# Kernel tuning notes

Measured on AMD Instinct MI355X. Metric: run time of the kernel, lower is better.

Reference implementation:

```python
import jax, jax.numpy as jnp
import numpy as np

FC = 8  # heads_count
EPS = 1e-12  # torch F.normalize eps


def setup_inputs() -> dict:
    key = jax.random.key(0)
    ks = jax.random.split(key, 8)
    n, l, s, C, H = 4, 4096, 256, 256, 256
    return {
        "x0": jax.random.normal(ks[0], (n, l, C), jnp.float32),
        "center1": jax.random.normal(ks[1], (n, s, C), jnp.float32),
        "W0": jax.random.normal(ks[2], (H, C), jnp.float32) * 0.05,
        "b0": jax.random.normal(ks[3], (H,), jnp.float32) * 0.05,
        "W1": jax.random.normal(ks[4], (2 * H, C), jnp.float32) * 0.05,
        "b1": jax.random.normal(ks[5], (2 * H,), jnp.float32) * 0.05,
        "Wm": jax.random.normal(ks[6], (C, H), jnp.float32) * 0.05,
        "bm": jax.random.normal(ks[7], (C,), jnp.float32) * 0.05,
        "alpha": jnp.ones((1,), jnp.float32),
        "beta": jnp.zeros((1,), jnp.float32),
    }


def _l2norm(x):
    # matches torch F.normalize(dim=-1): x / max(||x||, eps)
    nrm = jnp.sqrt(jnp.sum(x * x, axis=-1, keepdims=True))
    return x / jnp.maximum(nrm, EPS)


def reference(x0, center1, W0, b0, W1, b1, Wm, bm, alpha, beta):
    n, l, c = x0.shape
    s = center1.shape[1]
    H = W0.shape[0]
    sc = H // FC
    m = n * FC
    # projections
    x0p = x0 @ W0.T + b0                        # [n, l, H]
    c1 = center1 @ W1.T + b1                    # [n, s, 2H]
    # split heads: 'n l (fc sc) -> (n fc) l sc'
    x0p = x0p.reshape(n, l, FC, sc).transpose(0, 2, 1, 3).reshape(m, l, sc)
    c1 = c1.reshape(n, s, FC, 2 * sc).transpose(0, 2, 1, 3).reshape(m, s, 2 * sc)
    c_point, c_value = c1[..., :sc], c1[..., sc:]
    # cosine similarity + affine + sigmoid
    sim = jnp.einsum('mlc,msc->mls', _l2norm(x0p), _l2norm(c_point))
    sim = jax.nn.sigmoid(alpha[0] * sim + beta[0])
    # top-1 hard routing
    max_vals = jnp.max(sim, axis=2)             # [m, l]
    max_idx = jnp.argmax(sim, axis=2)           # [m, l]
    gathered = jnp.take_along_axis(c_value, max_idx[:, :, None], axis=1)  # [m, l, sc]
    dispatched = max_vals[:, :, None] * gathered
    # '(n fc) l sc -> n l (fc sc)'
    dispatched = dispatched.reshape(n, FC, l, sc).transpose(0, 2, 1, 3).reshape(n, l, H)
    return dispatched @ Wm.T + bm               # [n, l, c]
```

## Files before the change

### kernel.cpp

```cpp
#include <hip/hip_runtime.h>
#include <math.h>

#define Nn 4
#define Ll 4096
#define Ss 256
#define Cc 256
#define FC 8
#define SC 32

typedef __attribute__((ext_vector_type(8))) short short8;
typedef __attribute__((ext_vector_type(8))) _Float16 half8;
typedef __attribute__((ext_vector_type(4))) float f32x4;

__device__ __forceinline__ unsigned short f2bf(float x) {
  unsigned int u = __float_as_uint(x);
  return (unsigned short)((u + 0x7FFFu + ((u >> 16) & 1u)) >> 16);
}

__device__ __forceinline__ void split8v(float4 a, float4 b,
                                        half8& hi, half8& lo) {
  float v[8] = {a.x, a.y, a.z, a.w, b.x, b.y, b.z, b.w};
#pragma unroll
  for (int i = 0; i < 8; i++) {
    float x = v[i];
    _Float16 h = (_Float16)x;
    float r = (x - (float)h) * 2048.f;
    hi[i] = h;
    lo[i] = (_Float16)r;
  }
}

#define STAGE(Abuf, Bbuf, K0)                                               \
  {                                                                         \
    _Pragma("unroll")                                                       \
    for (int j = 0; j < 2; j++) {                                           \
      int c = wave * 2 + j;                                                 \
      const float* g = Ag + (m0blk + 8 * c + lr) * Cc + (K0) + scol;        \
      __builtin_amdgcn_global_load_lds(                                     \
          (const __attribute__((address_space(1))) void*)g,                 \
          (__attribute__((address_space(3))) void*)((Abuf) + c * 256),      \
          16, 0, 0);                                                        \
    }                                                                       \
    _Pragma("unroll")                                                       \
    for (int j = 0; j < 2; j++) {                                           \
      int c = wave * 2 + j;                                                 \
      const float* g =                                                      \
          Bg + (size_t)(n0blk + 8 * c + lr) * Cc + (K0) + scol;             \
      __builtin_amdgcn_global_load_lds(                                     \
          (const __attribute__((address_space(1))) void*)g,                 \
          (__attribute__((address_space(3))) void*)((Bbuf) + c * 256),      \
          16, 0, 0);                                                        \
    }                                                                       \
  }

#define KSTEP(Ac, Bc)                                                       \
  {                                                                         \
    half8 Bh[2], Bl[2];                                                     \
    _Pragma("unroll")                                                       \
    for (int ni = 0; ni < 2; ni++) {                                        \
      int rw = bR0 + ni * 16 + l15;                                         \
      int rb = rw * 32, xs = rw & 7;                                        \
      float4 f0 = *(const float4*)&(Bc)[rb + (((quad * 2) ^ xs) << 2)];     \
      float4 f1 = *(const float4*)&(Bc)[rb + (((quad * 2 + 1) ^ xs) << 2)]; \
      split8v(f0, f1, Bh[ni], Bl[ni]);                                      \
    }                                                                       \
    _Pragma("unroll")                                                       \
    for (int mi = 0; mi < 2; mi++) {                                        \
      int rw = aR0 + mi * 16 + l15;                                         \
      int rb = rw * 32, xs = rw & 7;                                        \
      float4 f0 = *(const float4*)&(Ac)[rb + (((quad * 2) ^ xs) << 2)];     \
      float4 f1 = *(const float4*)&(Ac)[rb + (((quad * 2 + 1) ^ xs) << 2)]; \
      half8 Ah, Al;                                                         \
      split8v(f0, f1, Ah, Al);                                              \
      _Pragma("unroll")                                                     \
      for (int ni = 0; ni < 2; ni++) {                                      \
        acc1[mi][ni] = __builtin_amdgcn_mfma_f32_16x16x32_f16(              \
            Ah, Bh[ni], acc1[mi][ni], 0, 0, 0);                             \
        acc2a[mi][ni] = __builtin_amdgcn_mfma_f32_16x16x32_f16(             \
            Ah, Bl[ni], acc2a[mi][ni], 0, 0, 0);                            \
        acc2b[mi][ni] = __builtin_amdgcn_mfma_f32_16x16x32_f16(             \
            Al, Bh[ni], acc2b[mi][ni], 0, 0, 0);                            \
      }                                                                     \
    }                                                                       \
  }

__global__ __launch_bounds__(256, 4) void proj_mfma_k(
    const float* __restrict__ x0, const float* __restrict__ W0,
    const float* __restrict__ b0, const float* __restrict__ center1,
    const float* __restrict__ W1, const float* __restrict__ b1,
    float* __restrict__ xn, float* __restrict__ cpn, float* __restrict__ cval) {
  __shared__ float As[2][64 * 32];
  __shared__ float Bs[2][64 * 32];
  int t = threadIdx.x;
  int wave = t >> 6, lane = t & 63;
  int quad = lane >> 4, l15 = lane & 15;
  int l8 = lane & 7, lr = lane >> 3;
  int scol = (l8 ^ lr) << 2;
  int b = blockIdx.x;

  const float *Ag, *Bg, *bias;
  size_t m0blk;
  int n0blk;
  bool isX = (b < 1024);
  if (isX) {
    int rt = b & 255, cb = b >> 8;
    m0blk = (size_t)rt * 64;
    n0blk = cb * 64;
    Ag = x0; Bg = W0; bias = b0;
  } else {
    int b2 = b - 1024;
    m0blk = (size_t)(b2 >> 3) * 64;
    n0blk = (b2 & 7) * 64;
    Ag = center1; Bg = W1; bias = b1;
  }

  int aR0 = (wave & 1) * 32;
  int bR0 = (wave >> 1) * 32;
  int n0w = n0blk + bR0;

  f32x4 acc1[2][2], acc2a[2][2], acc2b[2][2];
#pragma unroll
  for (int ni = 0; ni < 2; ni++) {
    float bv = bias[n0w + ni * 16 + l15];
    f32x4 ci = {bv, bv, bv, bv};
    f32x4 zz = {0.f, 0.f, 0.f, 0.f};
#pragma unroll
    for (int mi = 0; mi < 2; mi++) {
      acc1[mi][ni] = ci; acc2a[mi][ni] = zz; acc2b[mi][ni] = zz;
    }
  }

  float* Ac = &As[0][0]; float* An = &As[1][0];
  float* Bc = &Bs[0][0]; float* Bn = &Bs[1][0];
  STAGE(Ac, Bc, 0);
#pragma unroll 1
  for (int kt = 0; kt < 8; kt++) {
    if (kt < 7) {
      STAGE(An, Bn, (kt + 1) * 32);
      asm volatile("s_waitcnt vmcnt(4)" ::: "memory");
    } else {
      asm volatile("s_waitcnt vmcnt(0)" ::: "memory");
    }
    __builtin_amdgcn_sched_barrier(0);
    __builtin_amdgcn_s_barrier();
    __builtin_amdgcn_sched_barrier(0);
    KSTEP(Ac, Bc);
    asm volatile("s_waitcnt lgkmcnt(0)" ::: "memory");
    __builtin_amdgcn_sched_barrier(0);
    __builtin_amdgcn_s_barrier();
    __builtin_amdgcn_sched_barrier(0);
    float* tp;
    tp = Ac; Ac = An; An = tp;
    tp = Bc; Bc = Bn; Bn = tp;
  }

  size_t m0 = m0blk + aR0;
  if (isX) {
#pragma unroll
    for (int mi = 0; mi < 2; mi++) {
#pragma unroll
      for (int reg = 0; reg < 4; reg++) {
        size_t row = m0 + mi * 16 + quad * 4 + reg;
        float* orow = xn + row * Cc + n0w;
#pragma unroll
        for (int ni = 0; ni < 2; ni++)
          orow[ni * 16 + l15] =
              acc1[mi][ni][reg] +
              (acc2a[mi][ni][reg] + acc2b[mi][ni][reg]) * (1.f / 2048.f);
      }
    }
  } else {
    int f = n0w >> 6;
    bool point = (n0w & 32) == 0;
#pragma unroll
    for (int mi = 0; mi < 2; mi++) {
#pragma unroll
      for (int reg = 0; reg < 4; reg++) {
        int row = (int)m0 + mi * 16 + quad * 4 + reg;
        int nI = row >> 8, s = row & 255;
        float v0 = acc1[mi][0][reg] +
                   (acc2a[mi][0][reg] + acc2b[mi][0][reg]) * (1.f / 2048.f);
        float v1 = acc1[mi][1][reg] +
                   (acc2a[mi][1][reg] + acc2b[mi][1][reg]) * (1.f / 2048.f);
        size_t base = (((size_t)nI * FC + f) * Ss + s) * SC;
        if (point) {
          float ss = v0 * v0 + v1 * v1;
          ss += __shfl_xor(ss, 1, 64);
          ss += __shfl_xor(ss, 2, 64);
          ss += __shfl_xor(ss, 4, 64);
          ss += __shfl_xor(ss, 8, 64);
          float rin = 1.f / fmaxf(sqrtf(ss), 1e-12f);
          cpn[base + l15] = v0 * rin;
          cpn[base + 16 + l15] = v1 * rin;
        } else {
          cval[base + l15] = v0;
          cval[base + 16 + l15] = v1;
        }
      }
    }
  }
}

__global__ __launch_bounds__(256) void sim_k(
    float* __restrict__ xn, const float* __restrict__ cpn,
    const float* __restrict__ cval, const float* __restrict__ alphap,
    const float* __restrict__ betap) {
  __shared__ half8 BhS[4][256];
  __shared__ half8 BlS[4][256];
  int t = threadIdx.x;
  int wave = t >> 6, lane = t & 63;
  int quad = lane >> 4, l15 = lane & 15;
  int lt = blockIdx.x & 63;
  int nf = blockIdx.x >> 6;
  int f = nf & 7, nI = nf >> 3;
  int l0 = lt * 64;
  const float* cp = cpn + (size_t)nf * Ss * SC;

  {
    int s = t;
    float4 va[8];
#pragma unroll
    for (int q8 = 0; q8 < 8; q8++)
      va[q8] = *(const float4*)(cp + (size_t)s * SC + q8 * 4);
#pragma unroll
    for (int q = 0; q < 4; q++) {
      half8 h, l;
      split8v(va[2 * q], va[2 * q + 1], h, l);
      BhS[q][s] = h;
      BlS[q][s] = l;
    }
  }

  half8 Ah, Al;
  {
    const float* xrow =
        xn + ((size_t)nI * Ll + l0 + wave * 16 + l15) * Cc + f * SC + quad * 8;
    float4 a0 = *(const float4*)xrow;
    float4 a1 = *(const float4*)(xrow + 4);
    float ssq = a0.x * a0.x + a0.y * a0.y + a0.z * a0.z + a0.w * a0.w +
                a1.x * a1.x + a1.y * a1.y + a1.z * a1.z + a1.w * a1.w;
    ssq += __shfl_xor(ssq, 16, 64);
    ssq += __shfl_xor(ssq, 32, 64);
    float rin = 1.f / fmaxf(sqrtf(ssq), 1e-12f);
    a0.x *= rin; a0.y *= rin; a0.z *= rin; a0.w *= rin;
    a1.x *= rin; a1.y *= rin; a1.z *= rin; a1.w *= rin;
    split8v(a0, a1, Ah, Al);
  }

  __syncthreads();

  float a = alphap[0], bt = betap[0];
  float best[4];
  int bi[4];
#pragma unroll
  for (int r = 0; r < 4; r++) { best[r] = -3.0e38f; bi[r] = 0; }

#pragma unroll
  for (int j = 0; j < 16; j++) {
    half8 bh = BhS[quad][j * 16 + l15];
    half8 bl = BlS[quad][j * 16 + l15];
    f32x4 z = {0.f, 0.f, 0.f, 0.f};
    f32x4 c1 = __builtin_amdgcn_mfma_f32_16x16x32_f16(Ah, bh, z, 0, 0, 0);
    f32x4 c2 = __builtin_amdgcn_mfma_f32_16x16x32_f16(Ah, bl, z, 0, 0, 0);
    c2 = __builtin_amdgcn_mfma_f32_16x16x32_f16(Al, bh, c2, 0, 0, 0);
    int s = j * 16 + l15;
#pragma unroll
    for (int r = 0; r < 4; r++) {
      float v = c1[r] + c2[r] * (1.f / 2048.f);
      float tv = fmaf(a, v, bt);
      if (tv > best[r]) { best[r] = tv; bi[r] = s; }
    }
  }

#pragma unroll
  for (int r = 0; r < 4; r++) {
    float bv = best[r];
    int ix = bi[r];
#pragma unroll
    for (int m = 1; m <= 8; m <<= 1) {
      float ov = __shfl_xor(bv, m, 64);
      int oi = __shfl_xor(ix, m, 64);
      if (ov > bv || (ov == bv && oi < ix)) { bv = ov; ix = oi; }
    }
    float mv = 1.f / (1.f + expf(-bv));
    const float* cvp = cval + ((size_t)nf * Ss + ix) * SC;
    float* orow =
        xn + ((size_t)nI * Ll + l0 + wave * 16 + quad * 4 + r) * Cc + f * SC;
    orow[l15] = cvp[l15] * mv;
    orow[l15 + 16] = cvp[l15 + 16] * mv;
  }
}

__global__ __launch_bounds__(256) void out_mfma_k(
    const float* __restrict__ xn, const float* __restrict__ Wm,
    const float* __restrict__ bm, float* __restrict__ out) {
  int t = threadIdx.x;
  int wave = t >> 6, lane = t & 63;
  int quad = lane >> 4, l15 = lane & 15;
  size_t m0 = (size_t)(blockIdx.x >> 1) * 128 + (wave & 1) * 64;
  int n0 = (blockIdx.x & 1) * 128 + (wave >> 1) * 64;

  f32x4 acc[4][4];
#pragma unroll
  for (int ni = 0; ni < 4; ni++) {
    float bv = bm[n0 + ni * 16 + l15];
    f32x4 ci = {bv, bv, bv, bv};
#pragma unroll
    for (int mi = 0; mi < 4; mi++) acc[mi][ni] = ci;
  }

  for (int kt = 0; kt < 8; kt++) {
    int k0 = kt * 32 + quad * 8;
    short8 Af[4], Bf[4];
#pragma unroll
    for (int mi = 0; mi < 4; mi++) {
      const float* p = xn + (m0 + mi * 16 + l15) * Cc + k0;
      float4 lo = *(const float4*)p;
      float4 hi = *(const float4*)(p + 4);
      short8 fr;
      fr[0] = (short)f2bf(lo.x); fr[1] = (short)f2bf(lo.y);
      fr[2] = (short)f2bf(lo.z); fr[3] = (short)f2bf(lo.w);
      fr[4] = (short)f2bf(hi.x); fr[5] = (short)f2bf(hi.y);
      fr[6] = (short)f2bf(hi.z); fr[7] = (short)f2bf(hi.w);
      Af[mi] = fr;
    }
#pragma unroll
    for (int ni = 0; ni < 4; ni++) {
      const float* p = Wm + (size_t)(n0 + ni * 16 + l15) * Cc + k0;
      float4 lo = *(const float4*)p;
      float4 hi = *(const float4*)(p + 4);
      short8 fr;
      fr[0] = (short)f2bf(lo.x); fr[1] = (short)f2bf(lo.y);
      fr[2] = (short)f2bf(lo.z); fr[3] = (short)f2bf(lo.w);
      fr[4] = (short)f2bf(hi.x); fr[5] = (short)f2bf(hi.y);
      fr[6] = (short)f2bf(hi.z); fr[7] = (short)f2bf(hi.w);
      Bf[ni] = fr;
    }
#pragma unroll
    for (int mi = 0; mi < 4; mi++)
#pragma unroll
      for (int ni = 0; ni < 4; ni++)
        acc[mi][ni] = __builtin_amdgcn_mfma_f32_16x16x32_bf16(
            Af[mi], Bf[ni], acc[mi][ni], 0, 0, 0);
  }

#pragma unroll
  for (int mi = 0; mi < 4; mi++) {
#pragma unroll
    for (int reg = 0; reg < 4; reg++) {
      size_t row = m0 + mi * 16 + quad * 4 + reg;
      float* orow = out + row * Cc + n0;
#pragma unroll
      for (int ni = 0; ni < 4; ni++)
        orow[ni * 16 + l15] = acc[mi][ni][reg];
    }
  }
}

extern "C" void kernel_launch(void* const* d_in, const int* in_sizes, int n_in,
                              void* d_out, int out_size, void* d_ws, size_t ws_size,
                              hipStream_t stream) {
  const float* x0      = (const float*)d_in[0];
  const float* center1 = (const float*)d_in[1];
  const float* W0      = (const float*)d_in[2];
  const float* b0      = (const float*)d_in[3];
  const float* W1      = (const float*)d_in[4];
  const float* b1      = (const float*)d_in[5];
  const float* Wm      = (const float*)d_in[6];
  const float* bm      = (const float*)d_in[7];
  const float* alpha   = (const float*)d_in[8];
  const float* beta    = (const float*)d_in[9];
  float* out = (float*)d_out;
  float* ws  = (float*)d_ws;

  float* xn   = ws;
  float* cpn  = xn + (size_t)Nn * Ll * Cc;
  float* cval = cpn + (size_t)Nn * FC * Ss * SC;

  proj_mfma_k<<<dim3(1152), dim3(256), 0, stream>>>(
      x0, W0, b0, center1, W1, b1, xn, cpn, cval);
  sim_k<<<dim3(32 * 64), dim3(256), 0, stream>>>(xn, cpn, cval, alpha, beta);
  out_mfma_k<<<dim3(256), dim3(256), 0, stream>>>(xn, Wm, bm, out);
}
```

Before: 142.8 us.

## Use per-wave private LDS staging in projection and bf16 dispatch buffer

The projection kernel gives each wave its own double-buffered LDS region, so block-wide barriers are no longer needed; each wave stages the 32x32 A and B tiles it consumes itself. This duplicates global loads of shared tiles across waves and doubles LDS use per block, which may lower occupancy. Separately, the similarity kernel writes the dispatched result as bf16 into a new workspace buffer. The output GEMM then reads it directly as bf16 fragments, halving that traffic and removing the per-element conversion.

```diff
diff --git a/kernel.cpp b/kernel.cpp
--- a/kernel.cpp
+++ b/kernel.cpp
@@ -30,46 +30,43 @@
   }
 }
 
-#define STAGE(Abuf, Bbuf, K0)                                               \
+#define STAGE(Buf, K0)                                                      \
   {                                                                         \
     _Pragma("unroll")                                                       \
-    for (int j = 0; j < 2; j++) {                                           \
-      int c = wave * 2 + j;                                                 \
-      const float* g = Ag + (m0blk + 8 * c + lr) * Cc + (K0) + scol;        \
+    for (int c = 0; c < 4; c++) {                                           \
+      const float* g = Ag + (m0w + 8 * c + lr) * Cc + (K0) + scol;          \
       __builtin_amdgcn_global_load_lds(                                     \
           (const __attribute__((address_space(1))) void*)g,                 \
-          (__attribute__((address_space(3))) void*)((Abuf) + c * 256),      \
+          (__attribute__((address_space(3))) void*)((Buf) + c * 256),       \
           16, 0, 0);                                                        \
     }                                                                       \
     _Pragma("unroll")                                                       \
-    for (int j = 0; j < 2; j++) {                                           \
-      int c = wave * 2 + j;                                                 \
-      const float* g =                                                      \
-          Bg + (size_t)(n0blk + 8 * c + lr) * Cc + (K0) + scol;             \
+    for (int c = 0; c < 4; c++) {                                           \
+      const float* g = Bg + (size_t)(n0w + 8 * c + lr) * Cc + (K0) + scol;  \
       __builtin_amdgcn_global_load_lds(                                     \
           (const __attribute__((address_space(1))) void*)g,                 \
-          (__attribute__((address_space(3))) void*)((Bbuf) + c * 256),      \
+          (__attribute__((address_space(3))) void*)((Buf) + 1024 + c * 256),\
           16, 0, 0);                                                        \
     }                                                                       \
   }
 
-#define KSTEP(Ac, Bc)                                                       \
+#define KSTEP(Buf)                                                          \
   {                                                                         \
     half8 Bh[2], Bl[2];                                                     \
     _Pragma("unroll")                                                       \
     for (int ni = 0; ni < 2; ni++) {                                        \
-      int rw = bR0 + ni * 16 + l15;                                         \
-      int rb = rw * 32, xs = rw & 7;                                        \
-      float4 f0 = *(const float4*)&(Bc)[rb + (((quad * 2) ^ xs) << 2)];     \
-      float4 f1 = *(const float4*)&(Bc)[rb + (((quad * 2 + 1) ^ xs) << 2)]; \
+      int rw = ni * 16 + l15;                                               \
+      int rb = 1024 + rw * 32, xs = rw & 7;                                 \
+      float4 f0 = *(const float4*)&(Buf)[rb + (((quad * 2) ^ xs) << 2)];    \
+      float4 f1 = *(const float4*)&(Buf)[rb + (((quad * 2 + 1) ^ xs) << 2)];\
       split8v(f0, f1, Bh[ni], Bl[ni]);                                      \
     }                                                                       \
     _Pragma("unroll")                                                       \
     for (int mi = 0; mi < 2; mi++) {                                        \
-      int rw = aR0 + mi * 16 + l15;                                         \
+      int rw = mi * 16 + l15;                                               \
       int rb = rw * 32, xs = rw & 7;                                        \
-      float4 f0 = *(const float4*)&(Ac)[rb + (((quad * 2) ^ xs) << 2)];     \
-      float4 f1 = *(const float4*)&(Ac)[rb + (((quad * 2 + 1) ^ xs) << 2)]; \
+      float4 f0 = *(const float4*)&(Buf)[rb + (((quad * 2) ^ xs) << 2)];    \
+      float4 f1 = *(const float4*)&(Buf)[rb + (((quad * 2 + 1) ^ xs) << 2)];\
       half8 Ah, Al;                                                         \
       split8v(f0, f1, Ah, Al);                                              \
       _Pragma("unroll")                                                     \
@@ -84,13 +81,12 @@
     }                                                                       \
   }
 
-__global__ __launch_bounds__(256, 4) void proj_mfma_k(
+__global__ __launch_bounds__(256) void proj_mfma_k(
     const float* __restrict__ x0, const float* __restrict__ W0,
     const float* __restrict__ b0, const float* __restrict__ center1,
     const float* __restrict__ W1, const float* __restrict__ b1,
     float* __restrict__ xn, float* __restrict__ cpn, float* __restrict__ cval) {
-  __shared__ float As[2][64 * 32];
-  __shared__ float Bs[2][64 * 32];
+  __shared__ float P[4][2][2048];
   int t = threadIdx.x;
   int wave = t >> 6, lane = t & 63;
   int quad = lane >> 4, l15 = lane & 15;
@@ -114,9 +110,8 @@
     Ag = center1; Bg = W1; bias = b1;
   }
 
-  int aR0 = (wave & 1) * 32;
-  int bR0 = (wave >> 1) * 32;
-  int n0w = n0blk + bR0;
+  size_t m0w = m0blk + (size_t)(wave & 1) * 32;
+  int n0w = n0blk + (wave >> 1) * 32;
 
   f32x4 acc1[2][2], acc2a[2][2], acc2b[2][2];
 #pragma unroll
@@ -130,37 +125,29 @@
     }
   }
 
-  float* Ac = &As[0][0]; float* An = &As[1][0];
-  float* Bc = &Bs[0][0]; float* Bn = &Bs[1][0];
-  STAGE(Ac, Bc, 0);
+  float* B0p = &P[wave][0][0];
+  float* B1p = &P[wave][1][0];
+  STAGE(B0p, 0);
 #pragma unroll 1
   for (int kt = 0; kt < 8; kt++) {
+    float* cur = (kt & 1) ? B1p : B0p;
+    float* nxt = (kt & 1) ? B0p : B1p;
     if (kt < 7) {
-      STAGE(An, Bn, (kt + 1) * 32);
-      asm volatile("s_waitcnt vmcnt(4)" ::: "memory");
+      STAGE(nxt, (kt + 1) * 32);
+      asm volatile("s_waitcnt vmcnt(8)" ::: "memory");
     } else {
       asm volatile("s_waitcnt vmcnt(0)" ::: "memory");
     }
     __builtin_amdgcn_sched_barrier(0);
-    __builtin_amdgcn_s_barrier();
-    __builtin_amdgcn_sched_barrier(0);
-    KSTEP(Ac, Bc);
-    asm volatile("s_waitcnt lgkmcnt(0)" ::: "memory");
-    __builtin_amdgcn_sched_barrier(0);
-    __builtin_amdgcn_s_barrier();
-    __builtin_amdgcn_sched_barrier(0);
-    float* tp;
-    tp = Ac; Ac = An; An = tp;
-    tp = Bc; Bc = Bn; Bn = tp;
-  }
-
-  size_t m0 = m0blk + aR0;
+    KSTEP(cur);
+  }
+
   if (isX) {
 #pragma unroll
     for (int mi = 0; mi < 2; mi++) {
 #pragma unroll
       for (int reg = 0; reg < 4; reg++) {
-        size_t row = m0 + mi * 16 + quad * 4 + reg;
+        size_t row = m0w + mi * 16 + quad * 4 + reg;
         float* orow = xn + row * Cc + n0w;
 #pragma unroll
         for (int ni = 0; ni < 2; ni++)
@@ -176,7 +163,7 @@
     for (int mi = 0; mi < 2; mi++) {
 #pragma unroll
       for (int reg = 0; reg < 4; reg++) {
-        int row = (int)m0 + mi * 16 + quad * 4 + reg;
+        int row = (int)m0w + mi * 16 + quad * 4 + reg;
         int nI = row >> 8, s = row & 255;
         float v0 = acc1[mi][0][reg] +
                    (acc2a[mi][0][reg] + acc2b[mi][0][reg]) * (1.f / 2048.f);
@@ -202,9 +189,9 @@
 }
 
 __global__ __launch_bounds__(256) void sim_k(
-    float* __restrict__ xn, const float* __restrict__ cpn,
+    const float* __restrict__ xn, const float* __restrict__ cpn,
     const float* __restrict__ cval, const float* __restrict__ alphap,
-    const float* __restrict__ betap) {
+    const float* __restrict__ betap, unsigned short* __restrict__ xb) {
   __shared__ half8 BhS[4][256];
   __shared__ half8 BlS[4][256];
   int t = threadIdx.x;
@@ -284,15 +271,15 @@
     }
     float mv = 1.f / (1.f + expf(-bv));
     const float* cvp = cval + ((size_t)nf * Ss + ix) * SC;
-    float* orow =
-        xn + ((size_t)nI * Ll + l0 + wave * 16 + quad * 4 + r) * Cc + f * SC;
-    orow[l15] = cvp[l15] * mv;
-    orow[l15 + 16] = cvp[l15 + 16] * mv;
+    unsigned short* orow =
+        xb + ((size_t)nI * Ll + l0 + wave * 16 + quad * 4 + r) * Cc + f * SC;
+    orow[l15] = f2bf(cvp[l15] * mv);
+    orow[l15 + 16] = f2bf(cvp[l15 + 16] * mv);
   }
 }
 
 __global__ __launch_bounds__(256) void out_mfma_k(
-    const float* __restrict__ xn, const float* __restrict__ Wm,
+    const unsigned short* __restrict__ xb, const float* __restrict__ Wm,
     const float* __restrict__ bm, float* __restrict__ out) {
   int t = threadIdx.x;
   int wave = t >> 6, lane = t & 63;
@@ -313,17 +300,8 @@
     int k0 = kt * 32 + quad * 8;
     short8 Af[4], Bf[4];
 #pragma unroll
-    for (int mi = 0; mi < 4; mi++) {
-      const float* p = xn + (m0 + mi * 16 + l15) * Cc + k0;
-      float4 lo = *(const float4*)p;
-      float4 hi = *(const float4*)(p + 4);
-      short8 fr;
-      fr[0] = (short)f2bf(lo.x); fr[1] = (short)f2bf(lo.y);
-      fr[2] = (short)f2bf(lo.z); fr[3] = (short)f2bf(lo.w);
-      fr[4] = (short)f2bf(hi.x); fr[5] = (short)f2bf(hi.y);
-      fr[6] = (short)f2bf(hi.z); fr[7] = (short)f2bf(hi.w);
-      Af[mi] = fr;
-    }
+    for (int mi = 0; mi < 4; mi++)
+      Af[mi] = *(const short8*)(xb + (m0 + mi * 16 + l15) * Cc + k0);
 #pragma unroll
     for (int ni = 0; ni < 4; ni++) {
       const float* p = Wm + (size_t)(n0 + ni * 16 + l15) * Cc + k0;
@@ -376,9 +354,11 @@
   float* xn   = ws;
   float* cpn  = xn + (size_t)Nn * Ll * Cc;
   float* cval = cpn + (size_t)Nn * FC * Ss * SC;
+  unsigned short* xb =
+      (unsigned short*)(cval + (size_t)Nn * FC * Ss * SC);
 
   proj_mfma_k<<<dim3(1152), dim3(256), 0, stream>>>(
       x0, W0, b0, center1, W1, b1, xn, cpn, cval);
-  sim_k<<<dim3(32 * 64), dim3(256), 0, stream>>>(xn, cpn, cval, alpha, beta);
-  out_mfma_k<<<dim3(256), dim3(256), 0, stream>>>(xn, Wm, bm, out);
-}
+  sim_k<<<dim3(32 * 64), dim3(256), 0, stream>>>(xn, cpn, cval, alpha, beta, xb);
+  out_mfma_k<<<dim3(256), dim3(256), 0, stream>>>(xb, Wm, bm, out);
+}
```

New measurement: 148.4 us. 3.9% more time.
